# Kernel optimization log

Hardware: AMD Instinct MI355X
Metric: run time of the kernel (lower is better)

The kernel has to match this reference:

```python
import jax, jax.numpy as jnp
import numpy as np

INPUT_DIM = 128
DEPTH = 6
HIDDEN = 64
NUM_INNER = 2 ** DEPTH - 1  # 63
NUM_LEAVES = 2 ** DEPTH     # 64


def setup_inputs() -> dict:
    key = jax.random.key(0)
    ks = jax.random.split(key, 6)
    x = jax.random.normal(ks[0], (65536, INPUT_DIM), dtype=jnp.float32)
    s1 = 1.0 / np.sqrt(INPUT_DIM)
    s2 = 1.0 / np.sqrt(HIDDEN)
    W1 = jax.random.uniform(ks[1], (NUM_INNER, INPUT_DIM, HIDDEN), minval=-s1, maxval=s1, dtype=jnp.float32)
    b1 = jax.random.uniform(ks[2], (NUM_INNER, HIDDEN), minval=-s1, maxval=s1, dtype=jnp.float32)
    W2 = jax.random.uniform(ks[3], (NUM_INNER, HIDDEN), minval=-s2, maxval=s2, dtype=jnp.float32)
    b2 = jax.random.uniform(ks[4], (NUM_INNER,), minval=-s2, maxval=s2, dtype=jnp.float32)
    leaf = jax.random.normal(ks[5], (NUM_LEAVES, 1), dtype=jnp.float32)
    return {"x": x, "W1": W1, "b1": b1, "W2": W2, "b2": b2, "leaf": leaf}


def reference(x, W1, b1, W2, b2, leaf):
    # All inner-node MLPs as one batched GEMM pair: [B, N] node probabilities
    h = jax.nn.relu(jnp.einsum('bi,nih->bnh', x, W1) + b1)      # [B, N, H]
    probs = jax.nn.sigmoid(jnp.einsum('bnh,nh->bn', h, W2) + b2)  # [B, N]

    # Original code walks node_idx = 2*node_idx+1 unconditionally, so the chain
    # of used node indices is 2^k - 1 for k = 0..depth-1.
    chain = jnp.array([2 ** k - 1 for k in range(DEPTH)], dtype=jnp.int32)
    p_chain = probs[:, chain]  # [B, D]

    # Bit k (LSB first) of leaf index selects p (bit=1) vs 1-p (bit=0)
    leaves = np.arange(NUM_LEAVES)
    bits = jnp.asarray(((leaves[:, None] >> np.arange(DEPTH)[None, :]) & 1).astype(np.float32))  # [L, D]

    # path_probs[b, l] = prod_k ( bits[l,k]*p + (1-bits[l,k])*(1-p) )
    factors = bits[None, :, :] * p_chain[:, None, :] + (1.0 - bits[None, :, :]) * (1.0 - p_chain[:, None, :])  # [B, L, D]
    path_probs = jnp.prod(factors, axis=-1)  # [B, L]

    return (path_probs @ leaf)[:, 0]  # [B]
```

## Files before the change

### kernel.cpp

```cpp
#include <hip/hip_runtime.h>

typedef __attribute__((ext_vector_type(4))) float f32x4;
typedef __attribute__((ext_vector_type(8))) short bf16x8;
typedef __attribute__((ext_vector_type(4))) unsigned int u32x4;

#define IDIM    128
#define HID     64
#define TDEPTH  6
#define WROWS   32
#define NWAVES  8
#define BLOCK   (NWAVES * 64)
#define MROWS   (WROWS * NWAVES)
#define NODE_ELEMS 8192
#define WFRAG_ELEMS (TDEPTH * NODE_ELEMS)

__device__ __forceinline__ unsigned short f2bf(float f) {
    unsigned int u = __builtin_bit_cast(unsigned int, f);
    unsigned int r = (u + 0x7FFFu + ((u >> 16) & 1u)) >> 16;
    return (unsigned short)r;
}

__device__ __forceinline__ unsigned int f2bf_pk(float f0, float f1) {
    unsigned int u0 = __builtin_bit_cast(unsigned int, f0);
    unsigned int u1 = __builtin_bit_cast(unsigned int, f1);
    unsigned int t0 = u0 + 0x7FFFu + ((u0 >> 16) & 1u);
    unsigned int t1 = u1 + 0x7FFFu + ((u1 >> 16) & 1u);
    return (t1 & 0xFFFF0000u) | (t0 >> 16);
}

__global__ void prep_wfrag(const float* __restrict__ W1, unsigned short* __restrict__ wfrag) {
    int idx = blockIdx.x * 256 + threadIdx.x;
    if (idx >= WFRAG_ELEMS) return;
    int j    = idx & 7;
    int lane = (idx >> 3) & 63;
    int ct   = (idx >> 9) & 3;
    int ks   = (idx >> 11) & 3;
    int nd   = idx >> 13;
    int node = (1 << nd) - 1;
    int k    = ks * 32 + (lane >> 4) * 8 + j;
    int col  = ct * 16 + (lane & 15);
    wfrag[idx] = f2bf(W1[(node * IDIM + k) * HID + col]);
}

template <bool USE_WS>
__global__ __launch_bounds__(BLOCK, 2)
void sdt_kernel(const float* __restrict__ x, const float* __restrict__ W1,
                const float* __restrict__ b1, const float* __restrict__ W2,
                const float* __restrict__ b2, const float* __restrict__ leaf,
                const unsigned short* __restrict__ wfrag, float* __restrict__ out) {
    __shared__ __align__(16) unsigned short bs[3 * NODE_ELEMS];
    __shared__ float p_lds[NWAVES][WROWS][9];
    __shared__ float b1s[TDEPTH][HID];
    __shared__ float w2s[TDEPTH][HID];
    __shared__ float b2s[8];
    __shared__ float leaf_lds[64];

    const int tid  = threadIdx.x;
    const int wave = tid >> 6;
    const int lane = tid & 63;
    const int lcol = lane & 15;
    const int lq   = lane >> 4;
    const int m0   = blockIdx.x * MROWS + wave * WROWS;

    const float* xb = x + (size_t)(m0 + lcol) * IDIM + lq * 8;
    float4 araw[2][4][2];
    #pragma unroll
    for (int rt = 0; rt < 2; rt++)
        #pragma unroll
        for (int ks = 0; ks < 4; ks++) {
            const float4* ap = reinterpret_cast<const float4*>(
                xb + (size_t)(rt * 16) * IDIM + ks * 32);
            araw[rt][ks][0] = ap[0];
            araw[rt][ks][1] = ap[1];
        }

    auto stage3 = [&](int nd0) {
        if (USE_WS) {
            const u32x4* src = reinterpret_cast<const u32x4*>(
                wfrag + (size_t)nd0 * NODE_ELEMS);
            u32x4* dst = reinterpret_cast<u32x4*>(&bs[0]);
            #pragma unroll
            for (int i = 0; i < 6; i++)
                dst[tid + i * BLOCK] = src[tid + i * BLOCK];
        } else {
            for (int e = tid; e < 3 * NODE_ELEMS; e += BLOCK) {
                int j = e & 7, ln = (e >> 3) & 63, ct = (e >> 9) & 3,
                    ks = (e >> 11) & 3, ndl = e >> 13;
                int node = (1 << (nd0 + ndl)) - 1;
                int k    = ks * 32 + (ln >> 4) * 8 + j;
                int col  = ct * 16 + (ln & 15);
                bs[e] = f2bf(W1[((size_t)node * IDIM + k) * HID + col]);
            }
        }
    };

    stage3(0);
    if (tid < 384) {
        int nd = tid >> 6, col = tid & 63, node = (1 << nd) - 1;
        b1s[nd][col] = b1[node * HID + col];
        w2s[nd][col] = W2[node * HID + col];
    }
    if (tid < 6)  b2s[tid] = b2[(1 << tid) - 1];
    if (tid < 64) leaf_lds[tid] = leaf[tid];

    bf16x8 afrag[2][4];
    #pragma unroll
    for (int rt = 0; rt < 2; rt++)
        #pragma unroll
        for (int ks = 0; ks < 4; ks++) {
            float4 v0 = araw[rt][ks][0], v1 = araw[rt][ks][1];
            u32x4 pk;
            pk[0] = f2bf_pk(v0.x, v0.y);
            pk[1] = f2bf_pk(v0.z, v0.w);
            pk[2] = f2bf_pk(v1.x, v1.y);
            pk[3] = f2bf_pk(v1.z, v1.w);
            afrag[rt][ks] = __builtin_bit_cast(bf16x8, pk);
        }

    __syncthreads();

    auto compute = [&](int nd, int ndl) {
        f32x4 acc[2][4];
        #pragma unroll
        for (int rt = 0; rt < 2; rt++)
            #pragma unroll
            for (int ct = 0; ct < 4; ct++)
                acc[rt][ct] = (f32x4){0.f, 0.f, 0.f, 0.f};
        #pragma unroll
        for (int ks = 0; ks < 4; ks++) {
            bf16x8 bfrag[4];
            #pragma unroll
            for (int ct = 0; ct < 4; ct++)
                bfrag[ct] = *reinterpret_cast<const bf16x8*>(
                    &bs[ndl * NODE_ELEMS + (ks * 4 + ct) * 512 + lane * 8]);
            #pragma unroll
            for (int rt = 0; rt < 2; rt++)
                #pragma unroll
                for (int ct = 0; ct < 4; ct++)
                    acc[rt][ct] = __builtin_amdgcn_mfma_f32_16x16x32_bf16(
                        afrag[rt][ks], bfrag[ct], acc[rt][ct], 0, 0, 0);
        }

        float b1v[4], w2v[4];
        #pragma unroll
        for (int ct = 0; ct < 4; ct++) {
            b1v[ct] = b1s[nd][ct * 16 + lcol];
            w2v[ct] = w2s[nd][ct * 16 + lcol];
        }
        const float bias2 = b2s[nd];
        #pragma unroll
        for (int rt = 0; rt < 2; rt++) {
            #pragma unroll
            for (int r = 0; r < 4; r++) {
                float s = 0.f;
                #pragma unroll
                for (int ct = 0; ct < 4; ct++) {
                    float v = acc[rt][ct][r] + b1v[ct];
                    v = v > 0.f ? v : 0.f;
                    s += v * w2v[ct];
                }
                #pragma unroll
                for (int d = 1; d < 16; d <<= 1)
                    s += __shfl_xor(s, d, 64);
                float p = 1.f / (1.f + __expf(-(s + bias2)));
                if (lcol == 0)
                    p_lds[wave][rt * 16 + lq * 4 + r][nd] = p;
            }
        }
    };

    #pragma unroll 1
    for (int nd = 0; nd < 3; nd++) compute(nd, nd);
    __syncthreads();
    stage3(3);
    __syncthreads();
    #pragma unroll 1
    for (int nd = 3; nd < 6; nd++) compute(nd, nd - 3);
    __syncthreads();

    if (tid < MROWS) {
        const int wv = tid >> 5, row = tid & 31;
        float q0 = p_lds[wv][row][0];
        float q1 = p_lds[wv][row][1];
        float q2 = p_lds[wv][row][2];
        float q3 = p_lds[wv][row][3];
        float p4 = p_lds[wv][row][4];
        float p5 = p_lds[wv][row][5];
        float acc_out = 0.f;
        #pragma unroll
        for (int ch = 0; ch < 4; ch++) {
            float f4 = (ch & 1) ? p4 : 1.f - p4;
            float f5 = (ch & 2) ? p5 : 1.f - p5;
            const float* lf = leaf_lds + ch * 16;
            float tt[8];
            #pragma unroll
            for (int j = 0; j < 8; j++) {
                float a = lf[2 * j], b = lf[2 * j + 1];
                tt[j] = a + q0 * (b - a);
            }
            #pragma unroll
            for (int j = 0; j < 4; j++) tt[j] = tt[2 * j] + q1 * (tt[2 * j + 1] - tt[2 * j]);
            #pragma unroll
            for (int j = 0; j < 2; j++) tt[j] = tt[2 * j] + q2 * (tt[2 * j + 1] - tt[2 * j]);
            float s = tt[0] + q3 * (tt[1] - tt[0]);
            acc_out += f4 * f5 * s;
        }
        out[(size_t)blockIdx.x * MROWS + tid] = acc_out;
    }
}

extern "C" void kernel_launch(void* const* d_in, const int* in_sizes, int n_in,
                              void* d_out, int out_size, void* d_ws, size_t ws_size,
                              hipStream_t stream) {
    const float* x    = (const float*)d_in[0];
    const float* W1   = (const float*)d_in[1];
    const float* b1   = (const float*)d_in[2];
    const float* W2   = (const float*)d_in[3];
    const float* b2   = (const float*)d_in[4];
    const float* leaf = (const float*)d_in[5];
    float* out = (float*)d_out;

    const int Bn = in_sizes[0] / IDIM;
    const int nblocks = Bn / MROWS;

    if (ws_size >= (size_t)WFRAG_ELEMS * sizeof(unsigned short)) {
        unsigned short* wfrag = (unsigned short*)d_ws;
        prep_wfrag<<<(WFRAG_ELEMS + 255) / 256, 256, 0, stream>>>(W1, wfrag);
        sdt_kernel<true><<<nblocks, BLOCK, 0, stream>>>(x, W1, b1, W2, b2, leaf, wfrag, out);
    } else {
        sdt_kernel<false><<<nblocks, BLOCK, 0, stream>>>(x, W1, b1, W2, b2, leaf, nullptr, out);
    }
}
```

Before: 101.3 us.

## Swap MFMA operands so batch rows lie on lanes and stage all node weights once

The MFMA now takes weights as the A operand and x as the B operand, so each lane's accumulator holds hidden units for a single batch row. The hidden-dim reduction becomes an in-register sum plus two cross-lane shuffles, in place of a 16-lane butterfly per row. Node probabilities stay in registers, so the p_lds scratch buffer and the final block barrier are gone. All six nodes' weights are staged into LDS in one pass, which removes the mid-kernel restage and its two barriers. The cost is LDS use doubling to about 96KB, which may limit how many blocks fit per CU.

```diff
diff --git a/kernel.cpp b/kernel.cpp
--- a/kernel.cpp
+++ b/kernel.cpp
@@ -33,13 +33,13 @@
     if (idx >= WFRAG_ELEMS) return;
     int j    = idx & 7;
     int lane = (idx >> 3) & 63;
-    int ct   = (idx >> 9) & 3;
-    int ks   = (idx >> 11) & 3;
+    int ks   = (idx >> 9) & 3;
+    int ht   = (idx >> 11) & 3;
     int nd   = idx >> 13;
     int node = (1 << nd) - 1;
     int k    = ks * 32 + (lane >> 4) * 8 + j;
-    int col  = ct * 16 + (lane & 15);
-    wfrag[idx] = f2bf(W1[(node * IDIM + k) * HID + col]);
+    int hid  = ht * 16 + (lane & 15);
+    wfrag[idx] = f2bf(W1[((size_t)node * IDIM + k) * HID + hid]);
 }
 
 template <bool USE_WS>
@@ -48,8 +48,7 @@
                 const float* __restrict__ b1, const float* __restrict__ W2,
                 const float* __restrict__ b2, const float* __restrict__ leaf,
                 const unsigned short* __restrict__ wfrag, float* __restrict__ out) {
-    __shared__ __align__(16) unsigned short bs[3 * NODE_ELEMS];
-    __shared__ float p_lds[NWAVES][WROWS][9];
+    __shared__ __align__(16) unsigned short bs[TDEPTH * NODE_ELEMS];
     __shared__ float b1s[TDEPTH][HID];
     __shared__ float w2s[TDEPTH][HID];
     __shared__ float b2s[8];
@@ -65,127 +64,108 @@
     const float* xb = x + (size_t)(m0 + lcol) * IDIM + lq * 8;
     float4 araw[2][4][2];
     #pragma unroll
-    for (int rt = 0; rt < 2; rt++)
+    for (int bg = 0; bg < 2; bg++)
         #pragma unroll
         for (int ks = 0; ks < 4; ks++) {
             const float4* ap = reinterpret_cast<const float4*>(
-                xb + (size_t)(rt * 16) * IDIM + ks * 32);
-            araw[rt][ks][0] = ap[0];
-            araw[rt][ks][1] = ap[1];
-        }
-
-    auto stage3 = [&](int nd0) {
-        if (USE_WS) {
-            const u32x4* src = reinterpret_cast<const u32x4*>(
-                wfrag + (size_t)nd0 * NODE_ELEMS);
-            u32x4* dst = reinterpret_cast<u32x4*>(&bs[0]);
-            #pragma unroll
-            for (int i = 0; i < 6; i++)
-                dst[tid + i * BLOCK] = src[tid + i * BLOCK];
-        } else {
-            for (int e = tid; e < 3 * NODE_ELEMS; e += BLOCK) {
-                int j = e & 7, ln = (e >> 3) & 63, ct = (e >> 9) & 3,
-                    ks = (e >> 11) & 3, ndl = e >> 13;
-                int node = (1 << (nd0 + ndl)) - 1;
-                int k    = ks * 32 + (ln >> 4) * 8 + j;
-                int col  = ct * 16 + (ln & 15);
-                bs[e] = f2bf(W1[((size_t)node * IDIM + k) * HID + col]);
-            }
-        }
-    };
-
-    stage3(0);
-    if (tid < 384) {
-        int nd = tid >> 6, col = tid & 63, node = (1 << nd) - 1;
+                xb + (size_t)(bg * 16) * IDIM + ks * 32);
+            araw[bg][ks][0] = ap[0];
+            araw[bg][ks][1] = ap[1];
+        }
+
+    if (USE_WS) {
+        const u32x4* src = reinterpret_cast<const u32x4*>(wfrag);
+        u32x4* dst = reinterpret_cast<u32x4*>(&bs[0]);
+        #pragma unroll
+        for (int i = 0; i < (WFRAG_ELEMS * 2 / 16) / BLOCK; i++)
+            dst[tid + i * BLOCK] = src[tid + i * BLOCK];
+    } else {
+        for (int e = tid; e < WFRAG_ELEMS; e += BLOCK) {
+            int j = e & 7, ln = (e >> 3) & 63, ks = (e >> 9) & 3,
+                ht = (e >> 11) & 3, nd = e >> 13;
+            int node = (1 << nd) - 1;
+            int k    = ks * 32 + (ln >> 4) * 8 + j;
+            int hid  = ht * 16 + (ln & 15);
+            bs[e] = f2bf(W1[((size_t)node * IDIM + k) * HID + hid]);
+        }
+    }
+    for (int i = tid; i < TDEPTH * HID; i += BLOCK) {
+        int nd = i >> 6, col = i & 63, node = (1 << nd) - 1;
         b1s[nd][col] = b1[node * HID + col];
         w2s[nd][col] = W2[node * HID + col];
     }
     if (tid < 6)  b2s[tid] = b2[(1 << tid) - 1];
     if (tid < 64) leaf_lds[tid] = leaf[tid];
 
-    bf16x8 afrag[2][4];
-    #pragma unroll
-    for (int rt = 0; rt < 2; rt++)
+    bf16x8 xfrag[2][4];
+    #pragma unroll
+    for (int bg = 0; bg < 2; bg++)
         #pragma unroll
         for (int ks = 0; ks < 4; ks++) {
-            float4 v0 = araw[rt][ks][0], v1 = araw[rt][ks][1];
+            float4 v0 = araw[bg][ks][0], v1 = araw[bg][ks][1];
             u32x4 pk;
             pk[0] = f2bf_pk(v0.x, v0.y);
             pk[1] = f2bf_pk(v0.z, v0.w);
             pk[2] = f2bf_pk(v1.x, v1.y);
             pk[3] = f2bf_pk(v1.z, v1.w);
-            afrag[rt][ks] = __builtin_bit_cast(bf16x8, pk);
+            xfrag[bg][ks] = __builtin_bit_cast(bf16x8, pk);
         }
 
     __syncthreads();
 
-    auto compute = [&](int nd, int ndl) {
+    float pq[2][TDEPTH];
+
+    #pragma unroll
+    for (int nd = 0; nd < TDEPTH; nd++) {
         f32x4 acc[2][4];
         #pragma unroll
-        for (int rt = 0; rt < 2; rt++)
-            #pragma unroll
-            for (int ct = 0; ct < 4; ct++)
-                acc[rt][ct] = (f32x4){0.f, 0.f, 0.f, 0.f};
+        for (int bg = 0; bg < 2; bg++)
+            #pragma unroll
+            for (int ht = 0; ht < 4; ht++)
+                acc[bg][ht] = (f32x4){0.f, 0.f, 0.f, 0.f};
         #pragma unroll
         for (int ks = 0; ks < 4; ks++) {
-            bf16x8 bfrag[4];
-            #pragma unroll
-            for (int ct = 0; ct < 4; ct++)
-                bfrag[ct] = *reinterpret_cast<const bf16x8*>(
-                    &bs[ndl * NODE_ELEMS + (ks * 4 + ct) * 512 + lane * 8]);
-            #pragma unroll
-            for (int rt = 0; rt < 2; rt++)
+            bf16x8 awf[4];
+            #pragma unroll
+            for (int ht = 0; ht < 4; ht++)
+                awf[ht] = *reinterpret_cast<const bf16x8*>(
+                    &bs[(nd * 16 + ht * 4 + ks) * 512 + lane * 8]);
+            #pragma unroll
+            for (int bg = 0; bg < 2; bg++)
                 #pragma unroll
-                for (int ct = 0; ct < 4; ct++)
-                    acc[rt][ct] = __builtin_amdgcn_mfma_f32_16x16x32_bf16(
-                        afrag[rt][ks], bfrag[ct], acc[rt][ct], 0, 0, 0);
-        }
-
-        float b1v[4], w2v[4];
-        #pragma unroll
-        for (int ct = 0; ct < 4; ct++) {
-            b1v[ct] = b1s[nd][ct * 16 + lcol];
-            w2v[ct] = w2s[nd][ct * 16 + lcol];
+                for (int ht = 0; ht < 4; ht++)
+                    acc[bg][ht] = __builtin_amdgcn_mfma_f32_16x16x32_bf16(
+                        awf[ht], xfrag[bg][ks], acc[bg][ht], 0, 0, 0);
+        }
+
+        f32x4 b1q[4], w2q[4];
+        #pragma unroll
+        for (int ht = 0; ht < 4; ht++) {
+            b1q[ht] = *reinterpret_cast<const f32x4*>(&b1s[nd][ht * 16 + lq * 4]);
+            w2q[ht] = *reinterpret_cast<const f32x4*>(&w2s[nd][ht * 16 + lq * 4]);
         }
         const float bias2 = b2s[nd];
         #pragma unroll
-        for (int rt = 0; rt < 2; rt++) {
-            #pragma unroll
-            for (int r = 0; r < 4; r++) {
-                float s = 0.f;
+        for (int bg = 0; bg < 2; bg++) {
+            float s = 0.f;
+            #pragma unroll
+            for (int ht = 0; ht < 4; ht++)
                 #pragma unroll
-                for (int ct = 0; ct < 4; ct++) {
-                    float v = acc[rt][ct][r] + b1v[ct];
+                for (int r = 0; r < 4; r++) {
+                    float v = acc[bg][ht][r] + b1q[ht][r];
                     v = v > 0.f ? v : 0.f;
-                    s += v * w2v[ct];
+                    s += v * w2q[ht][r];
                 }
-                #pragma unroll
-                for (int d = 1; d < 16; d <<= 1)
-                    s += __shfl_xor(s, d, 64);
-                float p = 1.f / (1.f + __expf(-(s + bias2)));
-                if (lcol == 0)
-                    p_lds[wave][rt * 16 + lq * 4 + r][nd] = p;
-            }
-        }
-    };
-
-    #pragma unroll 1
-    for (int nd = 0; nd < 3; nd++) compute(nd, nd);
-    __syncthreads();
-    stage3(3);
-    __syncthreads();
-    #pragma unroll 1
-    for (int nd = 3; nd < 6; nd++) compute(nd, nd - 3);
-    __syncthreads();
-
-    if (tid < MROWS) {
-        const int wv = tid >> 5, row = tid & 31;
-        float q0 = p_lds[wv][row][0];
-        float q1 = p_lds[wv][row][1];
-        float q2 = p_lds[wv][row][2];
-        float q3 = p_lds[wv][row][3];
-        float p4 = p_lds[wv][row][4];
-        float p5 = p_lds[wv][row][5];
+            s += __shfl_xor(s, 16, 64);
+            s += __shfl_xor(s, 32, 64);
+            pq[bg][nd] = 1.f / (1.f + __expf(-(s + bias2)));
+        }
+    }
+
+    #pragma unroll
+    for (int bg = 0; bg < 2; bg++) {
+        float q0 = pq[bg][0], q1 = pq[bg][1], q2 = pq[bg][2];
+        float q3 = pq[bg][3], p4 = pq[bg][4], p5 = pq[bg][5];
         float acc_out = 0.f;
         #pragma unroll
         for (int ch = 0; ch < 4; ch++) {
@@ -205,7 +185,8 @@
             float s = tt[0] + q3 * (tt[1] - tt[0]);
             acc_out += f4 * f5 * s;
         }
-        out[(size_t)blockIdx.x * MROWS + tid] = acc_out;
+        if (lq == 0)
+            out[(size_t)m0 + bg * 16 + lcol] = acc_out;
     }
 }
 
```

Measured after the change: 94.04 us (median of 2 runs). -7.2%, faster.
